# Kernel tuning notes

Hardware: AMD Instinct MI355X
Metric: run time of the kernel (lower is better)

The kernel has to match this reference:

```python
import jax, jax.numpy as jnp
import numpy as np

WS = 8          # window_size
NH = 8          # num_heads
VD = 512        # values_dim
CD = 128        # coords_dim
INNER = 512     # inner_ratio * values_dim
E = INNER // NH # head_dim = 64
B, Hh, Ww_ = 2, 224, 224

# relative position indices (static)
_idx = np.array([[x, y] for x in range(WS) for y in range(WS)])
_rel = _idx[None, :, :] - _idx[:, None, :] + WS - 1  # (WS^2, WS^2, 2)
REL0 = jnp.asarray(_rel[:, :, 0])
REL1 = jnp.asarray(_rel[:, :, 1])

# shifted-window masks (static)
_s = WS * (WS // 2)
_rm = np.zeros((WS * WS, WS * WS), np.float32)
_rm[-_s:, :-_s] = -np.inf
_rm[:-_s, -_s:] = -np.inf
_cm = _rm.reshape(WS, WS, WS, WS).transpose(1, 0, 3, 2).reshape(WS * WS, WS * WS)
ROW_MASK = jnp.asarray(_rm)
COL_MASK = jnp.asarray(_cm)


def _rmsnorm(x, g, eps=1e-6):
    return x * g * jax.lax.rsqrt(jnp.mean(x * x, axis=-1, keepdims=True) + eps)


def _to_windows(x, b, Wh, Ww):
    # x: (b, hp, wp, INNER) with channel layout (e H) (head fastest)
    x = x.reshape(b, Wh, WS, Ww, WS, E, NH)
    return x.transpose(0, 6, 1, 3, 2, 4, 5).reshape(b, NH, Wh, Ww, WS * WS, E)


def setup_inputs() -> dict:
    key = jax.random.key(0)
    ks = jax.random.split(key, 8)
    s = 0.02
    return {
        "embedded_values": jax.random.normal(ks[0], (B, Hh, Ww_, VD), jnp.float32),
        "embedded_coords": jax.random.normal(ks[1], (B, Hh, Ww_, CD), jnp.float32),
        "Wqk_v": jax.random.normal(ks[2], (VD, 2 * INNER), jnp.float32) * s,
        "bqk_v": jnp.zeros((2 * INNER,), jnp.float32),
        "g_v": jnp.ones((2 * INNER,), jnp.float32),
        "Wv": jax.random.normal(ks[3], (VD, INNER), jnp.float32) * s,
        "bv": jnp.zeros((INNER,), jnp.float32),
        "Wqk_c": jax.random.normal(ks[4], (CD, 2 * INNER), jnp.float32) * s,
        "bqk_c": jnp.zeros((2 * INNER,), jnp.float32),
        "g_c": jnp.ones((2 * INNER,), jnp.float32),
        "pos_emb": jax.random.normal(ks[5], (2 * WS - 1, 2 * WS - 1), jnp.float32),
        "Wout": jax.random.normal(ks[6], (INNER, VD), jnp.float32) * s,
        "bout": jnp.zeros((VD,), jnp.float32),
    }


def reference(embedded_values, embedded_coords, Wqk_v, bqk_v, g_v, Wv, bv,
              Wqk_c, bqk_c, g_c, pos_emb, Wout, bout):
    b, h, w, _ = embedded_values.shape
    # projections; torch concat then rearrange '(d k)' k=3 interleaves channels -> reshape (..., INNER, 3)
    vqk = _rmsnorm(embedded_values @ Wqk_v + bqk_v, g_v)          # (b,h,w,2*INNER)
    vval = embedded_values @ Wv + bv                               # (b,h,w,INNER)
    v = jnp.concatenate([vqk, vval], axis=-1).reshape(b, h, w, INNER, 3)
    c = _rmsnorm(embedded_coords @ Wqk_c + bqk_c, g_c).reshape(b, h, w, INNER, 2)

    pad_h = (-h) % WS
    pad_w = (-w) % WS
    v = jnp.pad(v, ((0, 0), (0, pad_h), (0, pad_w), (0, 0), (0, 0)))
    c = jnp.pad(c, ((0, 0), (0, pad_h), (0, pad_w), (0, 0), (0, 0)))
    # shifted=True: roll windows by half window (no inverse roll in original)
    v = jnp.roll(v, (-(WS // 2), -(WS // 2)), axis=(1, 2))
    c = jnp.roll(c, (-(WS // 2), -(WS // 2)), axis=(1, 2))

    hp, wp = h + pad_h, w + pad_w
    Wh, Ww = hp // WS, wp // WS
    qv = _to_windows(v[..., 0], b, Wh, Ww)
    kv = _to_windows(v[..., 1], b, Wh, Ww)
    vv = _to_windows(v[..., 2], b, Wh, Ww)
    qc = _to_windows(c[..., 0], b, Wh, Ww)
    kc = _to_windows(c[..., 1], b, Wh, Ww)

    scale = float(E) ** 0.5
    dots = (jnp.einsum('bhijpe,bhijqe->bhijpq', qv, kv)
            + jnp.einsum('bhijpe,bhijqe->bhijpq', qc, kc)) / scale
    dots = dots + pos_emb[REL0, REL1]
    # shifted-window masks on last window row / column
    dots = dots.at[:, :, -1, :].add(ROW_MASK)
    dots = dots.at[:, :, :, -1].add(COL_MASK)

    attn = jax.nn.softmax(dots, axis=-1)
    y = jnp.einsum('bhijpq,bhijqe->bhijpe', attn, vv)
    # un-window; output channel layout is (H e) (head slow)
    y = y.reshape(b, NH, Wh, Ww, WS, WS, E).transpose(0, 2, 4, 3, 5, 1, 6)
    y = y.reshape(b, hp, wp, INNER)[:, :h, :w, :]
    return y @ Wout + bout
```

## Files before the change

kernel.cpp:

```cpp
#include <hip/hip_runtime.h>


using u16 = unsigned short;
typedef short bf16x8 __attribute__((ext_vector_type(8)));
typedef float f32x4 __attribute__((ext_vector_type(4)));
typedef u16 u16x4 __attribute__((ext_vector_type(4)));
typedef u16 u16x8 __attribute__((ext_vector_type(8)));

__device__ __forceinline__ float bf2f(u16 v) {
  return __uint_as_float(((unsigned)v) << 16);
}
__device__ __forceinline__ u16 f2bf(float f) {
  unsigned u = __float_as_uint(f);
  u += 0x7fffu + ((u >> 16) & 1u);
  return (u16)(u >> 16);
}

__device__ __forceinline__ void gld16(const u16* g, u16* l) {
  __builtin_amdgcn_global_load_lds(
      (const __attribute__((address_space(1))) unsigned*)g,
      (__attribute__((address_space(3))) unsigned*)l, 16, 0, 0);
}

struct f8 { float v[8]; };
__device__ __forceinline__ f8 ld8(const float* p) {
  f8 r;
  *(float4*)&r.v[0] = *(const float4*)p;
  *(float4*)&r.v[4] = *(const float4*)(p + 4);
  return r;
}
__device__ __forceinline__ bf16x8 nfrag(u16x8 raw, const f8& A, const f8& B, float s) {
  u16x8 o;
#pragma unroll
  for (int j = 0; j < 8; ++j) o[j] = f2bf(bf2f(raw[j]) * (A.v[j] * s + B.v[j]));
  return *(bf16x8*)&o;
}
__device__ __forceinline__ bf16x8 nfragA(u16x8 raw, const f8& A, float s) {
  u16x8 o;
#pragma unroll
  for (int j = 0; j < 8; ++j) o[j] = f2bf(bf2f(raw[j]) * (A.v[j] * s));
  return *(bf16x8*)&o;
}

__global__ void conv_bf16(const float* __restrict__ in, u16* __restrict__ out) {
  size_t i = ((size_t)blockIdx.x * 256 + threadIdx.x) * 8;
  float4 a = *(const float4*)(in + i);
  float4 b = *(const float4*)(in + i + 4);
  u16x8 o;
  o[0] = f2bf(a.x); o[1] = f2bf(a.y); o[2] = f2bf(a.z); o[3] = f2bf(a.w);
  o[4] = f2bf(b.x); o[5] = f2bf(b.y); o[6] = f2bf(b.z); o[7] = f2bf(b.w);
  *(u16x8*)(out + i) = o;
}

__global__ void prep_wv(const float* __restrict__ Wqkv, const float* __restrict__ Wv,
                        u16* __restrict__ out) {
  int idx = blockIdx.x * 256 + threadIdx.x;
  if (idx >= 1536 * 512) return;
  int j = idx >> 9, kk = idx & 511;
  int t = j >> 9, rr = j & 511, nn = rr >> 6, e = rr & 63;
  int cc = 3 * (e * 8 + nn) + t;
  float v = (cc < 1024) ? Wqkv[kk * 1024 + cc] : Wv[kk * 512 + (cc - 1024)];
  out[idx] = f2bf(v);
}

__global__ void prep_wc(const float* __restrict__ W, u16* __restrict__ out) {
  int idx = blockIdx.x * 256 + threadIdx.x;
  if (idx >= 1024 * 128) return;
  int j = idx >> 7, kk = idx & 127;
  int t = j >> 9, rr = j & 511, nn = rr >> 6, e = rr & 63;
  int cc = 2 * (e * 8 + nn) + t;
  out[idx] = f2bf(W[kk * 1024 + cc]);
}

__global__ void prep_wout(const float* __restrict__ W, u16* __restrict__ out) {
  int idx = blockIdx.x * 256 + threadIdx.x;
  if (idx >= 512 * 512) return;
  int o = idx >> 9, kk = idx & 511;
  out[idx] = f2bf(W[kk * 512 + o]);
}

__global__ void prep_vec(const float* __restrict__ bqkv, const float* __restrict__ g_v,
                         const float* __restrict__ bv, const float* __restrict__ bqkc,
                         const float* __restrict__ g_c,
                         float* __restrict__ bpv, float* __restrict__ gAv, float* __restrict__ gBv,
                         float* __restrict__ bpc, float* __restrict__ gAc, float* __restrict__ gBc) {
  int j = blockIdx.x * 256 + threadIdx.x;
  if (j < 1536) {
    int t = j >> 9, rr = j & 511, nn = rr >> 6, e = rr & 63;
    int cc = 3 * (e * 8 + nn) + t;
    if (cc < 1024) { bpv[j] = bqkv[cc]; gAv[j] = g_v[cc]; gBv[j] = 0.f; }
    else           { bpv[j] = bv[cc - 1024]; gAv[j] = 0.f; gBv[j] = 1.f; }
  }
  if (j < 1024) {
    int t = j >> 9, rr = j & 511, nn = rr >> 6, e = rr & 63;
    int cc = 2 * (e * 8 + nn) + t;
    bpc[j] = bqkc[cc]; gAc[j] = g_c[cc]; gBc[j] = 0.f;
  }
}

__global__ void prep_biasT(const float* __restrict__ pe, float* __restrict__ bT) {
  int idx = blockIdx.x * 256 + threadIdx.x;
  if (idx >= 4 * 4096) return;
  int v = idx >> 12, q = (idx >> 6) & 63, p = idx & 63;
  int ap = p >> 3, bp = p & 7, aq = q >> 3, bq = q & 7;
  float val = pe[(aq - ap + 7) * 15 + (bq - bp + 7)];
  if ((v & 1) && ((ap >= 4) != (aq >= 4))) val = -1e30f;
  if ((v & 2) && ((bp >= 4) != (bq >= 4))) val = -1e30f;
  bT[idx] = val;
}

template<int N, int K, int MODE>
__global__ __launch_bounds__(256, 4) void gemm_db(
    const u16* __restrict__ A, const u16* __restrict__ Bt,
    const float* __restrict__ bias, void* __restrict__ outp,
    float* __restrict__ part, const float* __restrict__ gB, int nwg) {
  constexpr int NCB = N / 128;
  constexpr int KT = K / 32;
  const int orig = blockIdx.x;
  const int work = (orig & 7) * (nwg >> 3) + (orig >> 3);
  const int bm = work / NCB, bn = work % NCB;

  const int tid = threadIdx.x;
  const int w = tid >> 6;
  const int lane = tid & 63;
  const int wr = w >> 1, wc = w & 1;
  const int g = lane >> 4, c = lane & 15;

  __shared__ u16 As[2 * 4096];
  __shared__ u16 Bs[2 * 4096];

  f32x4 acc[4][4] = {};
  const u16* Ag = A + (size_t)bm * 128 * K;
  const u16* Bg = Bt + (size_t)bn * 128 * K;

  auto stage = [&](int buf, int kt) {
    const int k0 = kt * 32;
#pragma unroll
    for (int i = 0; i < 2; ++i) {
      const int idx = i * 256 + tid;
      const int row = idx >> 2, ch = idx & 3;
      const int sch = ch ^ ((row >> 1) & 3);
      gld16(Ag + (size_t)row * K + k0 + sch * 8, As + buf * 4096 + idx * 8);
      gld16(Bg + (size_t)row * K + k0 + sch * 8, Bs + buf * 4096 + idx * 8);
    }
  };

  stage(0, 0);
  __syncthreads();

  const int swz = (c >> 1) & 3;
  for (int kt = 0; kt < KT; ++kt) {
    if (kt + 1 < KT) stage((kt + 1) & 1, kt + 1);
    const u16* Ab = As + (kt & 1) * 4096;
    const u16* Bb = Bs + (kt & 1) * 4096;
    bf16x8 af[4], bfv[4];
#pragma unroll
    for (int mi = 0; mi < 4; ++mi)
      af[mi] = *(const bf16x8*)(Ab + (wr * 64 + mi * 16 + c) * 32 + (g ^ swz) * 8);
#pragma unroll
    for (int ni = 0; ni < 4; ++ni)
      bfv[ni] = *(const bf16x8*)(Bb + (wc * 64 + ni * 16 + c) * 32 + (g ^ swz) * 8);
#pragma unroll
    for (int mi = 0; mi < 4; ++mi)
#pragma unroll
      for (int ni = 0; ni < 4; ++ni)
        acc[mi][ni] = __builtin_amdgcn_mfma_f32_16x16x32_bf16(bfv[ni], af[mi], acc[mi][ni], 0, 0, 0);
    __syncthreads();
  }

  const int rowbase = bm * 128 + wr * 64;
  const int colbase = bn * 128 + wc * 64;
  if constexpr (MODE == 0) {
    u16* O = (u16*)outp;
    float rowsq[4] = {0.f, 0.f, 0.f, 0.f};
#pragma unroll
    for (int ni = 0; ni < 4; ++ni) {
      const int col4 = colbase + ni * 16 + g * 4;
      const float4 bb = *(const float4*)(bias + col4);
      const float4 gb = *(const float4*)(gB + col4);
#pragma unroll
      for (int mi = 0; mi < 4; ++mi) {
        const int row = rowbase + mi * 16 + c;
        u16x4 pk;
        float v0 = acc[mi][ni][0] + bb.x;
        float v1 = acc[mi][ni][1] + bb.y;
        float v2 = acc[mi][ni][2] + bb.z;
        float v3 = acc[mi][ni][3] + bb.w;
        pk[0] = f2bf(v0); pk[1] = f2bf(v1); pk[2] = f2bf(v2); pk[3] = f2bf(v3);
        *(u16x4*)(O + (size_t)row * N + col4) = pk;
        rowsq[mi] += (gb.x == 0.f ? v0 * v0 : 0.f) + (gb.y == 0.f ? v1 * v1 : 0.f)
                   + (gb.z == 0.f ? v2 * v2 : 0.f) + (gb.w == 0.f ? v3 * v3 : 0.f);
      }
    }
#pragma unroll
    for (int mi = 0; mi < 4; ++mi) {
      float s = rowsq[mi];
      s += __shfl_xor(s, 16);
      s += __shfl_xor(s, 32);
      rowsq[mi] = s;
    }
    float* red = (float*)As;
    if (g == 0) {
#pragma unroll
      for (int mi = 0; mi < 4; ++mi)
        red[wc * 128 + wr * 64 + mi * 16 + c] = rowsq[mi];
    }
    __syncthreads();
    if (tid < 128)
      part[(size_t)(bm * 128 + tid) * NCB + bn] = red[tid] + red[128 + tid];
  } else {
    float* O = (float*)outp;
#pragma unroll
    for (int ni = 0; ni < 4; ++ni) {
      const int col4 = colbase + ni * 16 + g * 4;
      const float4 bb = *(const float4*)(bias + col4);
#pragma unroll
      for (int mi = 0; mi < 4; ++mi) {
        const int row = rowbase + mi * 16 + c;
        f32x4 o;
        o[0] = acc[mi][ni][0] + bb.x;
        o[1] = acc[mi][ni][1] + bb.y;
        o[2] = acc[mi][ni][2] + bb.z;
        o[3] = acc[mi][ni][3] + bb.w;
        *(f32x4*)(O + (size_t)row * N + col4) = o;
      }
    }
  }
}

template<int N, int K, int MODE>
__global__ __launch_bounds__(256) void gemm_sb(
    const u16* __restrict__ A, const u16* __restrict__ Bt,
    const float* __restrict__ bias, void* __restrict__ outp,
    float* __restrict__ part, const float* __restrict__ gB, int nwg) {
  constexpr int NCB = N / 128;
  constexpr int KT = K / 64;
  const int orig = blockIdx.x;
  const int work = (orig & 7) * (nwg >> 3) + (orig >> 3);
  const int bm = work / NCB, bn = work % NCB;

  const int tid = threadIdx.x;
  const int w = tid >> 6;
  const int lane = tid & 63;
  const int wr = w >> 1, wc = w & 1;
  const int g = lane >> 4, c = lane & 15;

  __shared__ u16 As[128 * 64];
  __shared__ u16 Bs[128 * 64];

  f32x4 acc[4][4] = {};
  const u16* Ag = A + (size_t)bm * 128 * K;
  const u16* Bg = Bt + (size_t)bn * 128 * K;

  auto stage = [&](int kt) {
    const int k0 = kt * 64;
#pragma unroll
    for (int i = 0; i < 4; ++i) {
      const int idx = i * 256 + tid;
      const int row = idx >> 3, p = idx & 7;
      const int q = p ^ (row & 7);
      gld16(Ag + (size_t)row * K + k0 + q * 8, As + idx * 8);
      gld16(Bg + (size_t)row * K + k0 + q * 8, Bs + idx * 8);
    }
  };

  const int cm = c & 7;
  for (int kt = 0; kt < KT; ++kt) {
    stage(kt);
    __syncthreads();
#pragma unroll
    for (int kk = 0; kk < 2; ++kk) {
      bf16x8 af[4], bfv[4];
#pragma unroll
      for (int mi = 0; mi < 4; ++mi)
        af[mi] = *(const bf16x8*)(As + (wr * 64 + mi * 16 + c) * 64 +
                                  ((4 * kk + g) ^ cm) * 8);
#pragma unroll
      for (int ni = 0; ni < 4; ++ni)
        bfv[ni] = *(const bf16x8*)(Bs + (wc * 64 + ni * 16 + c) * 64 +
                                   ((4 * kk + g) ^ cm) * 8);
#pragma unroll
      for (int mi = 0; mi < 4; ++mi)
#pragma unroll
        for (int ni = 0; ni < 4; ++ni)
          acc[mi][ni] = __builtin_amdgcn_mfma_f32_16x16x32_bf16(bfv[ni], af[mi], acc[mi][ni], 0, 0, 0);
    }
    __syncthreads();
  }

  const int rowbase = bm * 128 + wr * 64;
  const int colbase = bn * 128 + wc * 64;
  if constexpr (MODE == 0) {
    u16* O = (u16*)outp;
    float rowsq[4] = {0.f, 0.f, 0.f, 0.f};
#pragma unroll
    for (int ni = 0; ni < 4; ++ni) {
      const int col4 = colbase + ni * 16 + g * 4;
      const float4 bb = *(const float4*)(bias + col4);
      const float4 gb = *(const float4*)(gB + col4);
#pragma unroll
      for (int mi = 0; mi < 4; ++mi) {
        const int row = rowbase + mi * 16 + c;
        u16x4 pk;
        float v0 = acc[mi][ni][0] + bb.x;
        float v1 = acc[mi][ni][1] + bb.y;
        float v2 = acc[mi][ni][2] + bb.z;
        float v3 = acc[mi][ni][3] + bb.w;
        pk[0] = f2bf(v0); pk[1] = f2bf(v1); pk[2] = f2bf(v2); pk[3] = f2bf(v3);
        *(u16x4*)(O + (size_t)row * N + col4) = pk;
        rowsq[mi] += (gb.x == 0.f ? v0 * v0 : 0.f) + (gb.y == 0.f ? v1 * v1 : 0.f)
                   + (gb.z == 0.f ? v2 * v2 : 0.f) + (gb.w == 0.f ? v3 * v3 : 0.f);
      }
    }
#pragma unroll
    for (int mi = 0; mi < 4; ++mi) {
      float s = rowsq[mi];
      s += __shfl_xor(s, 16);
      s += __shfl_xor(s, 32);
      rowsq[mi] = s;
    }
    float* red = (float*)As;
    if (g == 0) {
#pragma unroll
      for (int mi = 0; mi < 4; ++mi)
        red[wc * 128 + wr * 64 + mi * 16 + c] = rowsq[mi];
    }
    __syncthreads();
    if (tid < 128)
      part[(size_t)(bm * 128 + tid) * NCB + bn] = red[tid] + red[128 + tid];
  } else {
    float* O = (float*)outp;
#pragma unroll
    for (int ni = 0; ni < 4; ++ni) {
      const int col4 = colbase + ni * 16 + g * 4;
      const float4 bb = *(const float4*)(bias + col4);
#pragma unroll
      for (int mi = 0; mi < 4; ++mi) {
        const int row = rowbase + mi * 16 + c;
        f32x4 o;
        o[0] = acc[mi][ni][0] + bb.x;
        o[1] = acc[mi][ni][1] + bb.y;
        o[2] = acc[mi][ni][2] + bb.z;
        o[3] = acc[mi][ni][3] + bb.w;
        *(f32x4*)(O + (size_t)row * N + col4) = o;
      }
    }
  }
}

__global__ void combine_scales(const float* __restrict__ pvp, const float* __restrict__ pcp,
                               float* __restrict__ sv, float* __restrict__ sc) {
  const int i = blockIdx.x * 256 + threadIdx.x;
  float s = 0.f;
#pragma unroll
  for (int k = 0; k < 12; ++k) s += pvp[(size_t)i * 12 + k];
  sv[i] = rsqrtf(s * (1.f / 1024.f) + 1e-6f);
  float s2 = 0.f;
#pragma unroll
  for (int k = 0; k < 8; ++k) s2 += pcp[(size_t)i * 8 + k];
  sc[i] = rsqrtf(s2 * (1.f / 1024.f) + 1e-6f);
}

__global__ __launch_bounds__(64) void attn_kernel(
    const u16* __restrict__ Pv, const u16* __restrict__ Pc,
    const float* __restrict__ sv, const float* __restrict__ sc,
    const float* __restrict__ gAv, const float* __restrict__ gBv,
    const float* __restrict__ gAc, const float* __restrict__ gBc,
    const float* __restrict__ biasT, u16* __restrict__ Y) {
  const int l = threadIdx.x;
  int bx = blockIdx.x;
  const int wj = bx % 28; bx /= 28;
  const int wi = bx % 28; bx /= 28;
  const int n = bx & 7;
  const int bi = bx >> 3;

  const int g = l >> 4, c = l & 15;
  const int rr0 = l >> 3, rch = l & 7;

  __shared__ u16 Vl[64 * 72];
  __shared__ u16 Pl[64 * 72];

  auto pixof = [&](int a, int b2) -> int {
    int y = wi * 8 + a + 4; if (y >= 224) y -= 224;
    int x = wj * 8 + b2 + 4; if (x >= 224) x -= 224;
    return (bi * 224 + y) * 224 + x;
  };

  int pixr[4]; float svr[4], scr[4];
#pragma unroll
  for (int r = 0; r < 4; ++r) {
    const int p = r * 16 + c;
    pixr[r] = pixof(p >> 3, p & 7);
    svr[r] = sv[pixr[r]];
    scr[r] = sc[pixr[r]];
  }

  u16x8 vreg[8]; float vs_[8];
#pragma unroll
  for (int i = 0; i < 8; ++i) {
    const int pix = pixof(i, rr0);
    vs_[i] = sv[pix];
    vreg[i] = *(const u16x8*)(Pv + (size_t)pix * 1536 + 1024 + n * 64 + rch * 8);
  }

  f32x4 acc[4][4] = {};
#pragma unroll
  for (int kk = 0; kk < 2; ++kk) {
    const int e0 = kk * 32 + g * 8;
    const f8 qA = ld8(gAv + n * 64 + e0), qB = ld8(gBv + n * 64 + e0);
    const f8 kA = ld8(gAv + 512 + n * 64 + e0), kB = ld8(gBv + 512 + n * 64 + e0);
    bf16x8 af[4], bq[4];
#pragma unroll
    for (int r = 0; r < 4; ++r) {
      const u16* src = Pv + (size_t)pixr[r] * 1536 + n * 64 + e0;
      af[r] = nfrag(*(const u16x8*)(src + 512), kA, kB, svr[r]);
      bq[r] = nfrag(*(const u16x8*)src, qA, qB, svr[r]);
    }
#pragma unroll
    for (int mi = 0; mi < 4; ++mi)
#pragma unroll
      for (int ni = 0; ni < 4; ++ni)
        acc[mi][ni] = __builtin_amdgcn_mfma_f32_16x16x32_bf16(af[mi], bq[ni], acc[mi][ni], 0, 0, 0);
  }
#pragma unroll
  for (int kk = 0; kk < 2; ++kk) {
    const int e0 = kk * 32 + g * 8;
    const f8 qA = ld8(gAc + n * 64 + e0);
    const f8 kA = ld8(gAc + 512 + n * 64 + e0);
    bf16x8 af[4], bq[4];
#pragma unroll
    for (int r = 0; r < 4; ++r) {
      const u16* src = Pc + (size_t)pixr[r] * 1024 + n * 64 + e0;
      af[r] = nfragA(*(const u16x8*)(src + 512), kA, scr[r]);
      bq[r] = nfragA(*(const u16x8*)src, qA, scr[r]);
    }
#pragma unroll
    for (int mi = 0; mi < 4; ++mi)
#pragma unroll
      for (int ni = 0; ni < 4; ++ni)
        acc[mi][ni] = __builtin_amdgcn_mfma_f32_16x16x32_bf16(af[mi], bq[ni], acc[mi][ni], 0, 0, 0);
  }

  const int variant = ((wi == 27) ? 1 : 0) | ((wj == 27) ? 2 : 0);
  const float* BT = biasT + variant * 4096;
#pragma unroll
  for (int mi = 0; mi < 4; ++mi)
#pragma unroll
    for (int ni = 0; ni < 4; ++ni)
#pragma unroll
      for (int r = 0; r < 4; ++r) {
        const int q = mi * 16 + g * 4 + r;
        const int p = ni * 16 + c;
        acc[mi][ni][r] = acc[mi][ni][r] * 0.125f + BT[q * 64 + p];
      }
  float rinv[4];
#pragma unroll
  for (int ni = 0; ni < 4; ++ni) {
    float m = -3.0e38f;
#pragma unroll
    for (int mi = 0; mi < 4; ++mi)
#pragma unroll
      for (int r = 0; r < 4; ++r) m = fmaxf(m, acc[mi][ni][r]);
    m = fmaxf(m, __shfl_xor(m, 16));
    m = fmaxf(m, __shfl_xor(m, 32));
    float ssum = 0.f;
#pragma unroll
    for (int mi = 0; mi < 4; ++mi)
#pragma unroll
      for (int r = 0; r < 4; ++r) {
        float e = __expf(acc[mi][ni][r] - m);
        acc[mi][ni][r] = e;
        ssum += e;
      }
    ssum += __shfl_xor(ssum, 16);
    ssum += __shfl_xor(ssum, 32);
    rinv[ni] = 1.f / ssum;
  }

#pragma unroll
  for (int mi = 0; mi < 4; ++mi)
#pragma unroll
    for (int ni = 0; ni < 4; ++ni) {
      u16x4 pk;
#pragma unroll
      for (int r = 0; r < 4; ++r) pk[r] = f2bf(acc[mi][ni][r] * rinv[ni]);
      *(u16x4*)(Pl + (ni * 16 + c) * 72 + mi * 16 + g * 4) = pk;
    }
  {
    const f8 vA = ld8(gAv + 1024 + n * 64 + rch * 8);
    const f8 vB = ld8(gBv + 1024 + n * 64 + rch * 8);
#pragma unroll
    for (int i = 0; i < 8; ++i) {
      bf16x8 nv = nfrag(vreg[i], vA, vB, vs_[i]);
      *(bf16x8*)(Vl + (i * 8 + rr0) * 72 + rch * 8) = nv;
    }
  }

  f32x4 ya[4][4] = {};
#pragma unroll
  for (int kk = 0; kk < 2; ++kk) {
    bf16x8 pa[4];
#pragma unroll
    for (int mi = 0; mi < 4; ++mi)
      pa[mi] = *(const bf16x8*)(Pl + (mi * 16 + c) * 72 + kk * 32 + g * 8);
#pragma unroll
    for (int ni = 0; ni < 4; ++ni) {
      u16x8 vtmp;
#pragma unroll
      for (int j = 0; j < 8; ++j)
        vtmp[j] = Vl[(kk * 32 + g * 8 + j) * 72 + ni * 16 + c];
      bf16x8 vb = *(bf16x8*)&vtmp;
#pragma unroll
      for (int mi = 0; mi < 4; ++mi)
        ya[mi][ni] = __builtin_amdgcn_mfma_f32_16x16x32_bf16(pa[mi], vb, ya[mi][ni], 0, 0, 0);
    }
  }

  u16* Yt = Pl;
#pragma unroll
  for (int mi = 0; mi < 4; ++mi)
#pragma unroll
    for (int ni = 0; ni < 4; ++ni) {
      u16x4 yk;
#pragma unroll
      for (int r = 0; r < 4; ++r) yk[r] = f2bf(ya[mi][ni][r]);
      *(u16x4*)(Yt + (ni * 16 + c) * 72 + mi * 16 + g * 4) = yk;
    }
#pragma unroll
  for (int it = 0; it < 8; ++it) {
    const int b2 = l >> 3;
    const int ch = l & 7;
    const int p = it * 8 + b2;
    u16x8 row;
#pragma unroll
    for (int j = 0; j < 8; ++j) row[j] = Yt[(ch * 8 + j) * 72 + p];
    const int oy = wi * 8 + it, ox = wj * 8 + b2;
    *(u16x8*)(Y + ((size_t)(bi * 224 + oy) * 224 + ox) * 512 + n * 64 + ch * 8) = row;
  }
}

extern "C" void kernel_launch(void* const* d_in, const int* in_sizes, int n_in,
                              void* d_out, int out_size, void* d_ws, size_t ws_size,
                              hipStream_t stream) {
  const float* ev   = (const float*)d_in[0];
  const float* ec   = (const float*)d_in[1];
  const float* Wqkv = (const float*)d_in[2];
  const float* bqkv = (const float*)d_in[3];
  const float* g_v  = (const float*)d_in[4];
  const float* Wv   = (const float*)d_in[5];
  const float* bv   = (const float*)d_in[6];
  const float* Wqkc = (const float*)d_in[7];
  const float* bqkc = (const float*)d_in[8];
  const float* g_c  = (const float*)d_in[9];
  const float* pe   = (const float*)d_in[10];
  const float* Wout = (const float*)d_in[11];
  const float* bout = (const float*)d_in[12];
  float* out = (float*)d_out;

  char* w = (char*)d_ws;
  auto take = [&](size_t b) { char* p = w; w += (b + 255) & ~(size_t)255; return p; };
  u16* Wvp   = (u16*)take(1536ull * 512 * 2);
  u16* Wcp   = (u16*)take(1024ull * 128 * 2);
  u16* Wob   = (u16*)take(512ull * 512 * 2);
  float* bpv = (float*)take(1536 * 4);
  float* gAv = (float*)take(1536 * 4);
  float* gBv = (float*)take(1536 * 4);
  float* bpc = (float*)take(1024 * 4);
  float* gAc = (float*)take(1024 * 4);
  float* gBc = (float*)take(1024 * 4);
  float* bT  = (float*)take(4 * 4096 * 4);
  u16* Pv    = (u16*)take(100352ull * 1536 * 2);
  u16* Pc    = (u16*)take(100352ull * 1024 * 2);
  float* pvp = (float*)take(100352ull * 12 * 4);
  float* pcp = (float*)take(100352ull * 8 * 4);
  float* sv  = (float*)take(100352ull * 4);
  float* sc  = (float*)take(100352ull * 4);
  u16* Yb    = (u16*)take(100352ull * 512 * 2);
  u16* evb   = Yb;
  u16* ecb   = (u16*)take(100352ull * 128 * 2);

  conv_bf16<<<25088, 256, 0, stream>>>(ev, evb);
  conv_bf16<<<6272, 256, 0, stream>>>(ec, ecb);
  prep_wv<<<3072, 256, 0, stream>>>(Wqkv, Wv, Wvp);
  prep_wc<<<512, 256, 0, stream>>>(Wqkc, Wcp);
  prep_wout<<<1024, 256, 0, stream>>>(Wout, Wob);
  prep_vec<<<6, 256, 0, stream>>>(bqkv, g_v, bv, bqkc, g_c, bpv, gAv, gBv, bpc, gAc, gBc);
  prep_biasT<<<64, 256, 0, stream>>>(pe, bT);

  gemm_db<1536, 512, 0><<<9408, 256, 0, stream>>>(evb, Wvp, bpv, Pv, pvp, gBv, 9408);
  gemm_sb<1024, 128, 0><<<6272, 256, 0, stream>>>(ecb, Wcp, bpc, Pc, pcp, gBc, 6272);
  combine_scales<<<392, 256, 0, stream>>>(pvp, pcp, sv, sc);
  attn_kernel<<<12544, 64, 0, stream>>>(Pv, Pc, sv, sc, gAv, gBv, gAc, gBc, bT, Yb);
  gemm_db<512, 512, 1><<<3136, 256, 0, stream>>>(Yb, Wob, bout, out, nullptr, nullptr, 3136);
}
```

Measured before the change: 742.4 us.

## Prefetch bias in fragment order, merge conversion launches, add MFMA priority hints

The relative-position bias table is re-laid out in per-lane fragment order, so each attention lane prefetches its 64 bias values with contiguous float4 loads before the QK matmul. This replaces scattered gathers after the MFMAs. The two fp32-to-bf16 conversion launches are merged into one grid, saving a kernel launch. s_setprio hints are placed around the MFMA blocks to favour matrix issue across waves. The cost is 64 extra registers per lane in the attention kernel, which may reduce occupancy.

Measured after the change: 763.0 us. +2.8%, slower.

```diff
diff --git a/kernel.cpp b/kernel.cpp
--- a/kernel.cpp
+++ b/kernel.cpp
@@ -42,13 +42,19 @@
   return *(bf16x8*)&o;
 }
 
-__global__ void conv_bf16(const float* __restrict__ in, u16* __restrict__ out) {
-  size_t i = ((size_t)blockIdx.x * 256 + threadIdx.x) * 8;
+__global__ void conv_bf16_2(const float* __restrict__ inA, u16* __restrict__ outA,
+                            const float* __restrict__ inB, u16* __restrict__ outB) {
+  int b = blockIdx.x;
+  const float* in;
+  u16* out;
+  size_t i;
+  if (b < 25088) { in = inA; out = outA; i = ((size_t)b * 256 + threadIdx.x) * 8; }
+  else           { in = inB; out = outB; i = ((size_t)(b - 25088) * 256 + threadIdx.x) * 8; }
   float4 a = *(const float4*)(in + i);
-  float4 b = *(const float4*)(in + i + 4);
+  float4 c = *(const float4*)(in + i + 4);
   u16x8 o;
   o[0] = f2bf(a.x); o[1] = f2bf(a.y); o[2] = f2bf(a.z); o[3] = f2bf(a.w);
-  o[4] = f2bf(b.x); o[5] = f2bf(b.y); o[6] = f2bf(b.z); o[7] = f2bf(b.w);
+  o[4] = f2bf(c.x); o[5] = f2bf(c.y); o[6] = f2bf(c.z); o[7] = f2bf(c.w);
   *(u16x8*)(out + i) = o;
 }
 
@@ -101,7 +107,10 @@
 __global__ void prep_biasT(const float* __restrict__ pe, float* __restrict__ bT) {
   int idx = blockIdx.x * 256 + threadIdx.x;
   if (idx >= 4 * 4096) return;
-  int v = idx >> 12, q = (idx >> 6) & 63, p = idx & 63;
+  int v = idx >> 12, l = (idx >> 6) & 63, j = idx & 63;
+  int g = l >> 4, c = l & 15;
+  int mi = j >> 4, ni = (j >> 2) & 3, r = j & 3;
+  int q = mi * 16 + g * 4 + r, p = ni * 16 + c;
   int ap = p >> 3, bp = p & 7, aq = q >> 3, bq = q & 7;
   float val = pe[(aq - ap + 7) * 15 + (bq - bp + 7)];
   if ((v & 1) && ((ap >= 4) != (aq >= 4))) val = -1e30f;
@@ -395,6 +404,13 @@
     scr[r] = sc[pixr[r]];
   }
 
+  const int variant = ((wi == 27) ? 1 : 0) | ((wj == 27) ? 2 : 0);
+  const float* BTL = biasT + variant * 4096 + l * 64;
+  float bt[64];
+#pragma unroll
+  for (int t = 0; t < 16; ++t)
+    *(float4*)&bt[t * 4] = *(const float4*)(BTL + t * 4);
+
   u16x8 vreg[8]; float vs_[8];
 #pragma unroll
   for (int i = 0; i < 8; ++i) {
@@ -416,11 +432,13 @@
       af[r] = nfrag(*(const u16x8*)(src + 512), kA, kB, svr[r]);
       bq[r] = nfrag(*(const u16x8*)src, qA, qB, svr[r]);
     }
+    __builtin_amdgcn_s_setprio(1);
 #pragma unroll
     for (int mi = 0; mi < 4; ++mi)
 #pragma unroll
       for (int ni = 0; ni < 4; ++ni)
         acc[mi][ni] = __builtin_amdgcn_mfma_f32_16x16x32_bf16(af[mi], bq[ni], acc[mi][ni], 0, 0, 0);
+    __builtin_amdgcn_s_setprio(0);
   }
 #pragma unroll
   for (int kk = 0; kk < 2; ++kk) {
@@ -434,25 +452,22 @@
       af[r] = nfragA(*(const u16x8*)(src + 512), kA, scr[r]);
       bq[r] = nfragA(*(const u16x8*)src, qA, scr[r]);
     }
+    __builtin_amdgcn_s_setprio(1);
 #pragma unroll
     for (int mi = 0; mi < 4; ++mi)
 #pragma unroll
       for (int ni = 0; ni < 4; ++ni)
         acc[mi][ni] = __builtin_amdgcn_mfma_f32_16x16x32_bf16(af[mi], bq[ni], acc[mi][ni], 0, 0, 0);
-  }
-
-  const int variant = ((wi == 27) ? 1 : 0) | ((wj == 27) ? 2 : 0);
-  const float* BT = biasT + variant * 4096;
+    __builtin_amdgcn_s_setprio(0);
+  }
+
 #pragma unroll
   for (int mi = 0; mi < 4; ++mi)
 #pragma unroll
     for (int ni = 0; ni < 4; ++ni)
 #pragma unroll
-      for (int r = 0; r < 4; ++r) {
-        const int q = mi * 16 + g * 4 + r;
-        const int p = ni * 16 + c;
-        acc[mi][ni][r] = acc[mi][ni][r] * 0.125f + BT[q * 64 + p];
-      }
+      for (int r = 0; r < 4; ++r)
+        acc[mi][ni][r] = acc[mi][ni][r] * 0.125f + bt[mi * 16 + ni * 4 + r];
   float rinv[4];
 #pragma unroll
   for (int ni = 0; ni < 4; ++ni) {
@@ -510,9 +525,11 @@
       for (int j = 0; j < 8; ++j)
         vtmp[j] = Vl[(kk * 32 + g * 8 + j) * 72 + ni * 16 + c];
       bf16x8 vb = *(bf16x8*)&vtmp;
+      __builtin_amdgcn_s_setprio(1);
 #pragma unroll
       for (int mi = 0; mi < 4; ++mi)
         ya[mi][ni] = __builtin_amdgcn_mfma_f32_16x16x32_bf16(pa[mi], vb, ya[mi][ni], 0, 0, 0);
+      __builtin_amdgcn_s_setprio(0);
     }
   }
 
@@ -579,8 +596,7 @@
   u16* evb   = Yb;
   u16* ecb   = (u16*)take(100352ull * 128 * 2);
 
-  conv_bf16<<<25088, 256, 0, stream>>>(ev, evb);
-  conv_bf16<<<6272, 256, 0, stream>>>(ec, ecb);
+  conv_bf16_2<<<31360, 256, 0, stream>>>(ev, evb, ec, ecb);
   prep_wv<<<3072, 256, 0, stream>>>(Wqkv, Wv, Wvp);
   prep_wc<<<512, 256, 0, stream>>>(Wqkc, Wcp);
   prep_wout<<<1024, 256, 0, stream>>>(Wout, Wob);
```

## Pre-normalize and transpose V into channel-major buffer for attention PV loads

Applied to the files above, without the earlier changes.

Adds a separate kernel that applies RMS-norm scaling to the V projection and writes it transposed as channel-major (channel, pixel) in global memory. The attention kernel then loads V MFMA B-fragments directly as 8 contiguous pixels per lane instead of staging V through shared memory with strided scalar reads. This removes per-window normalization and LDS transpose work but adds a full extra kernel pass that reads and writes about 100MB, plus a wrap-around split load for the last window column.

Result: slower. 852.4 us (+14.8%).

```diff
diff --git a/kernel.cpp b/kernel.cpp
--- a/kernel.cpp
+++ b/kernel.cpp
@@ -107,6 +107,37 @@
   if ((v & 1) && ((ap >= 4) != (aq >= 4))) val = -1e30f;
   if ((v & 2) && ((bp >= 4) != (bq >= 4))) val = -1e30f;
   bT[idx] = val;
+}
+
+__global__ __launch_bounds__(256) void vtrans(
+    const u16* __restrict__ Pv, const float* __restrict__ sv,
+    const float* __restrict__ gAv, const float* __restrict__ gBv,
+    u16* __restrict__ Vt) {
+  __shared__ u16 t[64 * 72];
+  const int tid = threadIdx.x;
+  const int p0 = blockIdx.x * 64;
+  const int c0 = blockIdx.y * 64;
+#pragma unroll
+  for (int it = 0; it < 2; ++it) {
+    const int idx = it * 256 + tid;
+    const int r = idx >> 3, ch = idx & 7;
+    const int pix = p0 + r;
+    const float s = sv[pix];
+    const f8 vA = ld8(gAv + 1024 + c0 + ch * 8);
+    const f8 vB = ld8(gBv + 1024 + c0 + ch * 8);
+    u16x8 raw = *(const u16x8*)(Pv + (size_t)pix * 1536 + 1024 + c0 + ch * 8);
+    *(bf16x8*)(t + r * 72 + ch * 8) = nfrag(raw, vA, vB, s);
+  }
+  __syncthreads();
+#pragma unroll
+  for (int it = 0; it < 2; ++it) {
+    const int idx = it * 256 + tid;
+    const int orow = idx >> 3, och = idx & 7;
+    u16x8 o;
+#pragma unroll
+    for (int j = 0; j < 8; ++j) o[j] = t[(och * 8 + j) * 72 + orow];
+    *(u16x8*)(Vt + (size_t)(c0 + orow) * 100352 + p0 + och * 8) = o;
+  }
 }
 
 template<int N, int K, int MODE>
@@ -363,6 +394,7 @@
 
 __global__ __launch_bounds__(64) void attn_kernel(
     const u16* __restrict__ Pv, const u16* __restrict__ Pc,
+    const u16* __restrict__ Vt,
     const float* __restrict__ sv, const float* __restrict__ sc,
     const float* __restrict__ gAv, const float* __restrict__ gBv,
     const float* __restrict__ gAc, const float* __restrict__ gBc,
@@ -375,9 +407,7 @@
   const int bi = bx >> 3;
 
   const int g = l >> 4, c = l & 15;
-  const int rr0 = l >> 3, rch = l & 7;
-
-  __shared__ u16 Vl[64 * 72];
+
   __shared__ u16 Pl[64 * 72];
 
   auto pixof = [&](int a, int b2) -> int {
@@ -393,14 +423,6 @@
     pixr[r] = pixof(p >> 3, p & 7);
     svr[r] = sv[pixr[r]];
     scr[r] = sc[pixr[r]];
-  }
-
-  u16x8 vreg[8]; float vs_[8];
-#pragma unroll
-  for (int i = 0; i < 8; ++i) {
-    const int pix = pixof(i, rr0);
-    vs_[i] = sv[pix];
-    vreg[i] = *(const u16x8*)(Pv + (size_t)pix * 1536 + 1024 + n * 64 + rch * 8);
   }
 
   f32x4 acc[4][4] = {};
@@ -486,30 +508,29 @@
       for (int r = 0; r < 4; ++r) pk[r] = f2bf(acc[mi][ni][r] * rinv[ni]);
       *(u16x4*)(Pl + (ni * 16 + c) * 72 + mi * 16 + g * 4) = pk;
     }
-  {
-    const f8 vA = ld8(gAv + 1024 + n * 64 + rch * 8);
-    const f8 vB = ld8(gBv + 1024 + n * 64 + rch * 8);
-#pragma unroll
-    for (int i = 0; i < 8; ++i) {
-      bf16x8 nv = nfrag(vreg[i], vA, vB, vs_[i]);
-      *(bf16x8*)(Vl + (i * 8 + rr0) * 72 + rch * 8) = nv;
-    }
-  }
 
   f32x4 ya[4][4] = {};
 #pragma unroll
   for (int kk = 0; kk < 2; ++kk) {
+    int y = wi * 8 + kk * 4 + g + 4; if (y >= 224) y -= 224;
+    const size_t rowoff = (size_t)bi * 50176 + (size_t)y * 224;
     bf16x8 pa[4];
 #pragma unroll
     for (int mi = 0; mi < 4; ++mi)
       pa[mi] = *(const bf16x8*)(Pl + (mi * 16 + c) * 72 + kk * 32 + g * 8);
 #pragma unroll
     for (int ni = 0; ni < 4; ++ni) {
-      u16x8 vtmp;
-#pragma unroll
-      for (int j = 0; j < 8; ++j)
-        vtmp[j] = Vl[(kk * 32 + g * 8 + j) * 72 + ni * 16 + c];
-      bf16x8 vb = *(bf16x8*)&vtmp;
+      const u16* vrow = Vt + (size_t)(n * 64 + ni * 16 + c) * 100352 + rowoff;
+      u16x8 vt;
+      if (wj != 27) {
+        vt = *(const u16x8*)(vrow + wj * 8 + 4);
+      } else {
+        u16x4 lo = *(const u16x4*)(vrow + 220);
+        u16x4 hi = *(const u16x4*)(vrow + 0);
+        vt[0] = lo[0]; vt[1] = lo[1]; vt[2] = lo[2]; vt[3] = lo[3];
+        vt[4] = hi[0]; vt[5] = hi[1]; vt[6] = hi[2]; vt[7] = hi[3];
+      }
+      bf16x8 vb = *(bf16x8*)&vt;
 #pragma unroll
       for (int mi = 0; mi < 4; ++mi)
         ya[mi][ni] = __builtin_amdgcn_mfma_f32_16x16x32_bf16(pa[mi], vb, ya[mi][ni], 0, 0, 0);
@@ -578,6 +599,7 @@
   u16* Yb    = (u16*)take(100352ull * 512 * 2);
   u16* evb   = Yb;
   u16* ecb   = (u16*)take(100352ull * 128 * 2);
+  u16* Vt    = (u16*)take(512ull * 100352 * 2);
 
   conv_bf16<<<25088, 256, 0, stream>>>(ev, evb);
   conv_bf16<<<6272, 256, 0, stream>>>(ec, ecb);
@@ -590,6 +612,7 @@
   gemm_db<1536, 512, 0><<<9408, 256, 0, stream>>>(evb, Wvp, bpv, Pv, pvp, gBv, 9408);
   gemm_sb<1024, 128, 0><<<6272, 256, 0, stream>>>(ecb, Wcp, bpc, Pc, pcp, gBc, 6272);
   combine_scales<<<392, 256, 0, stream>>>(pvp, pcp, sv, sc);
-  attn_kernel<<<12544, 64, 0, stream>>>(Pv, Pc, sv, sc, gAv, gBv, gAc, gBc, bT, Yb);
+  vtrans<<<dim3(1568, 8), 256, 0, stream>>>(Pv, sv, gAv, gBv, Vt);
+  attn_kernel<<<12544, 64, 0, stream>>>(Pv, Pc, Vt, sv, sc, gAv, gBv, gAc, gBc, bT, Yb);
   gemm_db<512, 512, 1><<<3136, 256, 0, stream>>>(Yb, Wob, bout, out, nullptr, nullptr, 3136);
 }
```
